# Kernel optimization log

Hardware: AMD Instinct MI355X
Metric: run time of the kernel (lower is better)

The kernel has to match this reference:

```python
import jax, jax.numpy as jnp
import numpy as np

DIM = 1024
HEADS = 16


def setup_inputs() -> dict:
    key = jax.random.key(0)
    k1, k2, k3, k4 = jax.random.split(key, 4)
    x = jax.random.normal(k1, (4, 2048, DIM), dtype=jnp.float32)
    # torch nn.Linear weights: [out_features, in_features]
    w_qkv = jax.random.normal(k2, (3 * DIM, DIM), dtype=jnp.float32) * (DIM ** -0.5)
    w_out = jax.random.normal(k3, (DIM, DIM), dtype=jnp.float32) * (DIM ** -0.5)
    b_out = jax.random.normal(k4, (DIM,), dtype=jnp.float32) * 0.01
    return {"x": x, "w_qkv": w_qkv, "w_out": w_out, "b_out": b_out}


def reference(x, w_qkv, w_out, b_out):
    b, n, d = x.shape
    h = HEADS
    hd = d // h
    scale = d ** -0.5  # note: full dim, matching the original module
    qkv = jnp.einsum('bnd,ed->bne', x, w_qkv)  # [b, n, 3d]
    q, k, v = jnp.split(qkv, 3, axis=-1)
    def to_heads(t):
        return t.reshape(b, n, h, hd).transpose(0, 2, 1, 3)  # [b, h, n, hd]
    q, k, v = map(to_heads, (q, k, v))
    dots = jnp.einsum('bhqd,bhkd->bhqk', q, k) * scale  # [b, h, n, n]
    attn = jax.nn.softmax(dots, axis=-1)
    out = jnp.einsum('bhqk,bhkd->bhqd', attn, v)  # [b, h, n, hd]
    out = out.transpose(0, 2, 1, 3).reshape(b, n, d)
    return jnp.einsum('bnd,ed->bne', out, w_out) + b_out
```

## Files before the change

### kernel.cpp

```cpp
#include <hip/hip_runtime.h>
#include <stdint.h>

#define SEQ   2048
#define NDIM  1024
#define NH    16
#define HD    64
#define KDIM  1024

typedef short  short8  __attribute__((ext_vector_type(8)));
typedef float  floatx4 __attribute__((ext_vector_type(4)));
typedef unsigned short ushort4v __attribute__((ext_vector_type(4)));
typedef _Float16 half8 __attribute__((ext_vector_type(8)));
typedef __fp16  fp16x2 __attribute__((ext_vector_type(2)));
typedef unsigned int uint2v __attribute__((ext_vector_type(2)));
typedef unsigned int uint4v __attribute__((ext_vector_type(4)));

typedef __attribute__((address_space(1))) void GV;
typedef __attribute__((address_space(3))) void LV;

#define QSCALE 0.04508422003f

__device__ __forceinline__ unsigned short f2bf(float f) {
    unsigned int u = __float_as_uint(f);
    u += 0x7fffu + ((u >> 16) & 1u);
    return (unsigned short)(u >> 16);
}

__device__ __forceinline__ float ex2(float x) {
#if __has_builtin(__builtin_amdgcn_exp2f)
    return __builtin_amdgcn_exp2f(x);
#else
    return exp2f(x);
#endif
}

__global__ __launch_bounds__(256) void cast_f32_bf16(const float* __restrict__ in,
                                                     unsigned short* __restrict__ out) {
    int i = (blockIdx.x * 256 + threadIdx.x) * 4;
    float4 v = *(const float4*)(in + i);
    ushort4v o;
    o.x = f2bf(v.x); o.y = f2bf(v.y); o.z = f2bf(v.z); o.w = f2bf(v.w);
    *(ushort4v*)(out + i) = o;
}

template<int MODE>
__global__ __launch_bounds__(256, 3)
void gemm_bt(const unsigned short* __restrict__ A,
             const unsigned short* __restrict__ B,
             unsigned short* __restrict__ Cq,
             unsigned short* __restrict__ Ck,
             unsigned short* __restrict__ Cv,
             const float* __restrict__ bias,
             float* __restrict__ Cout)
{
    __shared__ unsigned short As[2][4096];
    __shared__ unsigned short Bs[2][4096];
    const int tid  = threadIdx.x;
    const int lane = tid & 63;
    const int w    = tid >> 6;
    const int quad = lane >> 4;
    const int l15  = lane & 15;
    const int wm   = w >> 1, wn = w & 1;
    const int bm   = blockIdx.x, bn = blockIdx.y;

    const unsigned short* Arow = A + (size_t)bm * 128 * KDIM;
    const unsigned short* Brow = B + (size_t)bn * 128 * KDIM;

    const unsigned short* ga[2]; const unsigned short* gb[2];
    unsigned short* la[2][2];    unsigned short* lb[2][2];
#pragma unroll
    for (int i = 0; i < 2; ++i) {
        int j = ((w * 2 + i) << 6) + lane;
        int r = j >> 2;
        int c = (j & 3) ^ ((r >> 1) & 3);
        ga[i] = Arow + r * KDIM + c * 8;
        gb[i] = Brow + r * KDIM + c * 8;
#pragma unroll
        for (int b = 0; b < 2; ++b) {
            la[b][i] = &As[b][(w * 2 + i) << 9];
            lb[b][i] = &Bs[b][(w * 2 + i) << 9];
        }
    }

    int achunk[4], bchunk[4];
#pragma unroll
    for (int t = 0; t < 4; ++t) {
        int ra = wm * 64 + t * 16 + l15;
        achunk[t] = (ra << 2) + (quad ^ ((ra >> 1) & 3));
        int rb = wn * 64 + t * 16 + l15;
        bchunk[t] = (rb << 2) + (quad ^ ((rb >> 1) & 3));
    }

    floatx4 acc[4][4];
#pragma unroll
    for (int mt = 0; mt < 4; ++mt)
#pragma unroll
        for (int nt = 0; nt < 4; ++nt)
            acc[mt][nt] = (floatx4){0.f, 0.f, 0.f, 0.f};

#pragma unroll
    for (int i = 0; i < 2; ++i) {
        __builtin_amdgcn_global_load_lds((GV*)(void*)ga[i], (LV*)(void*)la[0][i], 16, 0, 0);
        __builtin_amdgcn_global_load_lds((GV*)(void*)gb[i], (LV*)(void*)lb[0][i], 16, 0, 0);
    }

    for (int kt = 0; kt < KDIM / 32; ++kt) {
        const int buf = kt & 1;
        __syncthreads();
        if (kt < KDIM / 32 - 1) {
#pragma unroll
            for (int i = 0; i < 2; ++i) {
                __builtin_amdgcn_global_load_lds((GV*)(void*)(ga[i] + (kt + 1) * 32), (LV*)(void*)la[buf ^ 1][i], 16, 0, 0);
                __builtin_amdgcn_global_load_lds((GV*)(void*)(gb[i] + (kt + 1) * 32), (LV*)(void*)lb[buf ^ 1][i], 16, 0, 0);
            }
        }
        short8 af[4], bf[4];
#pragma unroll
        for (int t = 0; t < 4; ++t) {
            af[t] = *(const short8*)(&As[buf][0] + (achunk[t] << 3));
            bf[t] = *(const short8*)(&Bs[buf][0] + (bchunk[t] << 3));
        }
#pragma unroll
        for (int mt = 0; mt < 4; ++mt)
#pragma unroll
            for (int nt = 0; nt < 4; ++nt)
                acc[mt][nt] = __builtin_amdgcn_mfma_f32_16x16x32_bf16(af[mt], bf[nt], acc[mt][nt], 0, 0, 0);
    }

    if (MODE == 0) {
        const int which = bn >> 3;
        unsigned short* dst = which == 0 ? Cq : (which == 1 ? Ck : Cv);
        if (which == 2) {
#pragma unroll
            for (int nt = 0; nt < 4; ++nt) {
                int e0   = ((bn & 7) << 7) + wn * 64 + nt * 16;
                int head = e0 >> 6;
                int hdi  = (e0 & 63) + l15;
#pragma unroll
                for (int mt = 0; mt < 4; ++mt) {
                    int n0 = bm * 128 + wm * 64 + mt * 16 + quad * 4;
                    int b  = n0 >> 11;
                    int n  = n0 & 2047;
                    int bh = (b << 4) + head;
                    int u  = (n & 127) >> 5;
                    size_t base = (size_t)bh * 131072
                                + (size_t)(n >> 7) * 8192
                                + (size_t)(u * 4 + ((hdi >> 4) & 3)) * 512
                                + (quad * 16 + (hdi & 15)) * 8
                                + ((mt & 1) << 2);
                    fp16x2 p01 = __builtin_amdgcn_cvt_pkrtz(acc[mt][nt][0], acc[mt][nt][1]);
                    fp16x2 p23 = __builtin_amdgcn_cvt_pkrtz(acc[mt][nt][2], acc[mt][nt][3]);
                    uint2v st;
                    st.x = __builtin_bit_cast(unsigned int, p01);
                    st.y = __builtin_bit_cast(unsigned int, p23);
                    *(uint2v*)(dst + base) = st;
                }
            }
        } else {
#pragma unroll
            for (int nt = 0; nt < 4; ++nt) {
                int e0   = ((bn & 7) << 7) + wn * 64 + nt * 16;
                int head = e0 >> 6;
                int hdi  = (e0 & 63) + l15;
#pragma unroll
                for (int mt = 0; mt < 4; ++mt) {
#pragma unroll
                    for (int r = 0; r < 4; ++r) {
                        int m = bm * 128 + wm * 64 + mt * 16 + quad * 4 + r;
                        int b = m >> 11, n = m & 2047;
                        int bh = (b << 4) + head;
                        float val = acc[mt][nt][r];
                        if (which == 0) {
                            dst[((size_t)bh * SEQ + n) * HD + hdi] = f2bf(val * QSCALE);
                        } else {
                            size_t idx = (size_t)bh * 131072
                                       + (size_t)(n >> 7) * 8192
                                       + (size_t)((((n >> 4) & 7) * 2) + (hdi >> 5)) * 512
                                       + ((((hdi >> 3) & 3) * 16) + (n & 15)) * 8
                                       + (hdi & 7);
                            dst[idx] = f2bf(val);
                        }
                    }
                }
            }
        }
    } else {
#pragma unroll
        for (int nt = 0; nt < 4; ++nt) {
            int e = bn * 128 + wn * 64 + nt * 16 + l15;
            float bv = bias[e];
#pragma unroll
            for (int mt = 0; mt < 4; ++mt) {
#pragma unroll
                for (int r = 0; r < 4; ++r) {
                    int m = bm * 128 + wm * 64 + mt * 16 + quad * 4 + r;
                    Cout[(size_t)m * NDIM + e] = acc[mt][nt][r] + bv;
                }
            }
        }
    }
}

__global__ __launch_bounds__(256, 4)
void attn_fused(const unsigned short* __restrict__ qb,
                const unsigned short* __restrict__ kfrag,
                const unsigned short* __restrict__ vfrag,
                unsigned short* __restrict__ ob)
{
    __shared__ unsigned short Ks[2][4096];
    __shared__ unsigned short Vs[2][4096];

    const int tid  = threadIdx.x;
    const int lane = tid & 63;
    const int w    = tid >> 6;
    const int quad = lane >> 4;
    const int l15  = lane & 15;

    const int bid  = blockIdx.x;
    const int xcd  = bid & 7;
    const int slot = bid >> 3;
    const int bh   = xcd * 8 + (slot >> 4);
    const int q0   = (slot & 15) * 128;

    const unsigned short* Qb = qb    + (size_t)bh * SEQ * HD;
    const unsigned short* Kb = kfrag + (size_t)bh * 131072;
    const unsigned short* Vb = vfrag + (size_t)bh * 131072;

    short8 qf[2][2];
#pragma unroll
    for (int qt = 0; qt < 2; ++qt)
#pragma unroll
        for (int ks = 0; ks < 2; ++ks)
            qf[qt][ks] = *(const short8*)(Qb + (size_t)(q0 + w * 32 + qt * 16 + l15) * HD + ks * 32 + quad * 8);

    floatx4 oacc[2][4];
    floatx4 lacc4[2];
#pragma unroll
    for (int qt = 0; qt < 2; ++qt) {
#pragma unroll
        for (int nt = 0; nt < 4; ++nt) oacc[qt][nt] = (floatx4){0.f, 0.f, 0.f, 0.f};
        lacc4[qt] = (floatx4){0.f, 0.f, 0.f, 0.f};
    }
    half8 vones;
#pragma unroll
    for (int i = 0; i < 8; ++i) vones[i] = (_Float16)1.0f;

    const unsigned short* gk[2]; const unsigned short* gv[2];
    unsigned short* lk[2][2];    unsigned short* lv[2][2];
#pragma unroll
    for (int i = 0; i < 2; ++i) {
        int off = (((w * 2 + i) << 6) + lane) * 8;
        gk[i] = Kb + off;
        gv[i] = Vb + off;
#pragma unroll
        for (int b = 0; b < 2; ++b) {
            lk[b][i] = &Ks[b][(w * 2 + i) << 9];
            lv[b][i] = &Vs[b][(w * 2 + i) << 9];
        }
    }

#pragma unroll
    for (int i = 0; i < 2; ++i) {
        __builtin_amdgcn_global_load_lds((GV*)(void*)gk[i], (LV*)(void*)lk[0][i], 16, 0, 0);
        __builtin_amdgcn_global_load_lds((GV*)(void*)gv[i], (LV*)(void*)lv[0][i], 16, 0, 0);
    }

    for (int t = 0; t < 32; ++t) {
        const int buf = t & 1;
        __syncthreads();
        if (t < 31) {
#pragma unroll
            for (int i = 0; i < 2; ++i) {
                __builtin_amdgcn_global_load_lds((GV*)(void*)(gk[i] + (t + 1) * 4096), (LV*)(void*)lk[buf ^ 1][i], 16, 0, 0);
                __builtin_amdgcn_global_load_lds((GV*)(void*)(gv[i] + (t + 1) * 4096), (LV*)(void*)lv[buf ^ 1][i], 16, 0, 0);
            }
        }
        const unsigned short* KsB = Ks[buf];
        const unsigned short* VsB = Vs[buf];

        floatx4 sacc[2][4];
#pragma unroll
        for (int qt = 0; qt < 2; ++qt)
#pragma unroll
            for (int nt = 0; nt < 4; ++nt) sacc[qt][nt] = (floatx4){0.f, 0.f, 0.f, 0.f};
#pragma unroll
        for (int ks = 0; ks < 2; ++ks) {
#pragma unroll
            for (int nt = 0; nt < 4; ++nt) {
                short8 kf = *(const short8*)(KsB + (nt * 2 + ks) * 512 + lane * 8);
                sacc[0][nt] = __builtin_amdgcn_mfma_f32_16x16x32_bf16(kf, qf[0][ks], sacc[0][nt], 0, 0, 0);
                sacc[1][nt] = __builtin_amdgcn_mfma_f32_16x16x32_bf16(kf, qf[1][ks], sacc[1][nt], 0, 0, 0);
            }
        }

#pragma unroll
        for (int u = 0; u < 2; ++u) {
            half8 pf[2];
#pragma unroll
            for (int qt = 0; qt < 2; ++qt) {
                floatx4 s0 = sacc[qt][2 * u];
                floatx4 s1 = sacc[qt][2 * u + 1];
                fp16x2 c0 = __builtin_amdgcn_cvt_pkrtz(ex2(s0[0]), ex2(s0[1]));
                fp16x2 c1 = __builtin_amdgcn_cvt_pkrtz(ex2(s0[2]), ex2(s0[3]));
                fp16x2 c2 = __builtin_amdgcn_cvt_pkrtz(ex2(s1[0]), ex2(s1[1]));
                fp16x2 c3 = __builtin_amdgcn_cvt_pkrtz(ex2(s1[2]), ex2(s1[3]));
                uint4v uu;
                uu.x = __builtin_bit_cast(unsigned int, c0);
                uu.y = __builtin_bit_cast(unsigned int, c1);
                uu.z = __builtin_bit_cast(unsigned int, c2);
                uu.w = __builtin_bit_cast(unsigned int, c3);
                pf[qt] = __builtin_bit_cast(half8, uu);
                lacc4[qt] = __builtin_amdgcn_mfma_f32_16x16x32_f16(pf[qt], vones, lacc4[qt], 0, 0, 0);
            }
#pragma unroll
            for (int nt = 0; nt < 4; ++nt) {
                uint4v vv = *(const uint4v*)(VsB + (u * 4 + nt) * 512 + lane * 8);
                half8 vf = __builtin_bit_cast(half8, vv);
                oacc[0][nt] = __builtin_amdgcn_mfma_f32_16x16x32_f16(pf[0], vf, oacc[0][nt], 0, 0, 0);
                oacc[1][nt] = __builtin_amdgcn_mfma_f32_16x16x32_f16(pf[1], vf, oacc[1][nt], 0, 0, 0);
            }
        }
    }

    const int b = bh >> 4, h = bh & 15;
#pragma unroll
    for (int qt = 0; qt < 2; ++qt) {
#pragma unroll
        for (int r = 0; r < 4; ++r) {
            float inv = 1.f / lacc4[qt][r];
            int n = q0 + w * 32 + qt * 16 + quad * 4 + r;
            size_t rowoff = ((size_t)b * SEQ + n) * NDIM + h * HD;
#pragma unroll
            for (int nt = 0; nt < 4; ++nt)
                ob[rowoff + nt * 16 + l15] = f2bf(oacc[qt][nt][r] * inv);
        }
    }
}

extern "C" void kernel_launch(void* const* d_in, const int* in_sizes, int n_in,
                              void* d_out, int out_size, void* d_ws, size_t ws_size,
                              hipStream_t stream)
{
    (void)in_sizes; (void)n_in; (void)out_size; (void)ws_size;
    const float* x    = (const float*)d_in[0];
    const float* wqkv = (const float*)d_in[1];
    const float* wout = (const float*)d_in[2];
    const float* bout = (const float*)d_in[3];
    float* out = (float*)d_out;

    unsigned short* xb    = (unsigned short*)d_ws;
    unsigned short* wqkvb = xb    + 8388608;
    unsigned short* woutb = wqkvb + 3145728;
    unsigned short* qbuf  = woutb + 1048576;
    unsigned short* kbuf  = qbuf  + 8388608;
    unsigned short* vbuf  = kbuf  + 8388608;
    unsigned short* obuf  = vbuf  + 8388608;

    cast_f32_bf16<<<8192, 256, 0, stream>>>(x, xb);
    cast_f32_bf16<<<3072, 256, 0, stream>>>(wqkv, wqkvb);
    cast_f32_bf16<<<1024, 256, 0, stream>>>(wout, woutb);

    gemm_bt<0><<<dim3(64, 24), 256, 0, stream>>>(xb, wqkvb, qbuf, kbuf, vbuf, nullptr, nullptr);
    attn_fused<<<1024, 256, 0, stream>>>(qbuf, kbuf, vbuf, obuf);
    gemm_bt<1><<<dim3(64, 8), 256, 0, stream>>>(obuf, woutb, nullptr, nullptr, nullptr, bout, out);
}
```

Before: 264.1 us.

## Split attention block across eight waves of sixteen query rows each

The attention kernel now launches 512 threads per block instead of 256. Each wave owns 16 query rows instead of 32, and each wave issues one K and one V async global-to-LDS copy per tile instead of two. Register use per wave roughly halves and launch bounds are raised to allow more resident waves, with s_setprio raised around the MFMA bursts to favour matrix issue. In exchange, every K/V fragment read from LDS now feeds half as many MFMAs, so LDS read traffic per FLOP doubles, and the tighter register cap may cause spills.

New measurement: 270.3 us. 2.3% more time.

```diff
diff --git a/kernel.cpp b/kernel.cpp
--- a/kernel.cpp
+++ b/kernel.cpp
@@ -201,7 +201,7 @@
     }
 }
 
-__global__ __launch_bounds__(256, 4)
+__global__ __launch_bounds__(512, 8)
 void attn_fused(const unsigned short* __restrict__ qb,
                 const unsigned short* __restrict__ kfrag,
                 const unsigned short* __restrict__ vfrag,
@@ -226,114 +226,89 @@
     const unsigned short* Kb = kfrag + (size_t)bh * 131072;
     const unsigned short* Vb = vfrag + (size_t)bh * 131072;
 
-    short8 qf[2][2];
-#pragma unroll
-    for (int qt = 0; qt < 2; ++qt)
-#pragma unroll
-        for (int ks = 0; ks < 2; ++ks)
-            qf[qt][ks] = *(const short8*)(Qb + (size_t)(q0 + w * 32 + qt * 16 + l15) * HD + ks * 32 + quad * 8);
-
-    floatx4 oacc[2][4];
-    floatx4 lacc4[2];
-#pragma unroll
-    for (int qt = 0; qt < 2; ++qt) {
-#pragma unroll
-        for (int nt = 0; nt < 4; ++nt) oacc[qt][nt] = (floatx4){0.f, 0.f, 0.f, 0.f};
-        lacc4[qt] = (floatx4){0.f, 0.f, 0.f, 0.f};
-    }
+    short8 qf[2];
+#pragma unroll
+    for (int ks = 0; ks < 2; ++ks)
+        qf[ks] = *(const short8*)(Qb + (size_t)(q0 + w * 16 + l15) * HD + ks * 32 + quad * 8);
+
+    floatx4 oacc[4];
+#pragma unroll
+    for (int nt = 0; nt < 4; ++nt) oacc[nt] = (floatx4){0.f, 0.f, 0.f, 0.f};
+    floatx4 lacc = (floatx4){0.f, 0.f, 0.f, 0.f};
+
     half8 vones;
 #pragma unroll
     for (int i = 0; i < 8; ++i) vones[i] = (_Float16)1.0f;
 
-    const unsigned short* gk[2]; const unsigned short* gv[2];
-    unsigned short* lk[2][2];    unsigned short* lv[2][2];
-#pragma unroll
-    for (int i = 0; i < 2; ++i) {
-        int off = (((w * 2 + i) << 6) + lane) * 8;
-        gk[i] = Kb + off;
-        gv[i] = Vb + off;
-#pragma unroll
-        for (int b = 0; b < 2; ++b) {
-            lk[b][i] = &Ks[b][(w * 2 + i) << 9];
-            lv[b][i] = &Vs[b][(w * 2 + i) << 9];
-        }
-    }
-
-#pragma unroll
-    for (int i = 0; i < 2; ++i) {
-        __builtin_amdgcn_global_load_lds((GV*)(void*)gk[i], (LV*)(void*)lk[0][i], 16, 0, 0);
-        __builtin_amdgcn_global_load_lds((GV*)(void*)gv[i], (LV*)(void*)lv[0][i], 16, 0, 0);
-    }
+    const unsigned short* gk = Kb + (size_t)((w << 6) + lane) * 8;
+    const unsigned short* gv = Vb + (size_t)((w << 6) + lane) * 8;
+    unsigned short* lk[2] = { &Ks[0][w << 9], &Ks[1][w << 9] };
+    unsigned short* lv[2] = { &Vs[0][w << 9], &Vs[1][w << 9] };
+
+    __builtin_amdgcn_global_load_lds((GV*)(void*)gk, (LV*)(void*)lk[0], 16, 0, 0);
+    __builtin_amdgcn_global_load_lds((GV*)(void*)gv, (LV*)(void*)lv[0], 16, 0, 0);
 
     for (int t = 0; t < 32; ++t) {
         const int buf = t & 1;
         __syncthreads();
         if (t < 31) {
-#pragma unroll
-            for (int i = 0; i < 2; ++i) {
-                __builtin_amdgcn_global_load_lds((GV*)(void*)(gk[i] + (t + 1) * 4096), (LV*)(void*)lk[buf ^ 1][i], 16, 0, 0);
-                __builtin_amdgcn_global_load_lds((GV*)(void*)(gv[i] + (t + 1) * 4096), (LV*)(void*)lv[buf ^ 1][i], 16, 0, 0);
-            }
+            __builtin_amdgcn_global_load_lds((GV*)(void*)(gk + (t + 1) * 4096), (LV*)(void*)lk[buf ^ 1], 16, 0, 0);
+            __builtin_amdgcn_global_load_lds((GV*)(void*)(gv + (t + 1) * 4096), (LV*)(void*)lv[buf ^ 1], 16, 0, 0);
         }
         const unsigned short* KsB = Ks[buf];
         const unsigned short* VsB = Vs[buf];
 
-        floatx4 sacc[2][4];
-#pragma unroll
-        for (int qt = 0; qt < 2; ++qt)
-#pragma unroll
-            for (int nt = 0; nt < 4; ++nt) sacc[qt][nt] = (floatx4){0.f, 0.f, 0.f, 0.f};
+        floatx4 sacc[4];
+#pragma unroll
+        for (int nt = 0; nt < 4; ++nt) sacc[nt] = (floatx4){0.f, 0.f, 0.f, 0.f};
+
+        __builtin_amdgcn_s_setprio(1);
 #pragma unroll
         for (int ks = 0; ks < 2; ++ks) {
 #pragma unroll
             for (int nt = 0; nt < 4; ++nt) {
                 short8 kf = *(const short8*)(KsB + (nt * 2 + ks) * 512 + lane * 8);
-                sacc[0][nt] = __builtin_amdgcn_mfma_f32_16x16x32_bf16(kf, qf[0][ks], sacc[0][nt], 0, 0, 0);
-                sacc[1][nt] = __builtin_amdgcn_mfma_f32_16x16x32_bf16(kf, qf[1][ks], sacc[1][nt], 0, 0, 0);
-            }
-        }
+                sacc[nt] = __builtin_amdgcn_mfma_f32_16x16x32_bf16(kf, qf[ks], sacc[nt], 0, 0, 0);
+            }
+        }
+        __builtin_amdgcn_s_setprio(0);
 
 #pragma unroll
         for (int u = 0; u < 2; ++u) {
-            half8 pf[2];
-#pragma unroll
-            for (int qt = 0; qt < 2; ++qt) {
-                floatx4 s0 = sacc[qt][2 * u];
-                floatx4 s1 = sacc[qt][2 * u + 1];
-                fp16x2 c0 = __builtin_amdgcn_cvt_pkrtz(ex2(s0[0]), ex2(s0[1]));
-                fp16x2 c1 = __builtin_amdgcn_cvt_pkrtz(ex2(s0[2]), ex2(s0[3]));
-                fp16x2 c2 = __builtin_amdgcn_cvt_pkrtz(ex2(s1[0]), ex2(s1[1]));
-                fp16x2 c3 = __builtin_amdgcn_cvt_pkrtz(ex2(s1[2]), ex2(s1[3]));
-                uint4v uu;
-                uu.x = __builtin_bit_cast(unsigned int, c0);
-                uu.y = __builtin_bit_cast(unsigned int, c1);
-                uu.z = __builtin_bit_cast(unsigned int, c2);
-                uu.w = __builtin_bit_cast(unsigned int, c3);
-                pf[qt] = __builtin_bit_cast(half8, uu);
-                lacc4[qt] = __builtin_amdgcn_mfma_f32_16x16x32_f16(pf[qt], vones, lacc4[qt], 0, 0, 0);
-            }
+            floatx4 s0 = sacc[2 * u];
+            floatx4 s1 = sacc[2 * u + 1];
+            fp16x2 c0 = __builtin_amdgcn_cvt_pkrtz(ex2(s0[0]), ex2(s0[1]));
+            fp16x2 c1 = __builtin_amdgcn_cvt_pkrtz(ex2(s0[2]), ex2(s0[3]));
+            fp16x2 c2 = __builtin_amdgcn_cvt_pkrtz(ex2(s1[0]), ex2(s1[1]));
+            fp16x2 c3 = __builtin_amdgcn_cvt_pkrtz(ex2(s1[2]), ex2(s1[3]));
+            uint4v uu;
+            uu.x = __builtin_bit_cast(unsigned int, c0);
+            uu.y = __builtin_bit_cast(unsigned int, c1);
+            uu.z = __builtin_bit_cast(unsigned int, c2);
+            uu.w = __builtin_bit_cast(unsigned int, c3);
+            half8 pf = __builtin_bit_cast(half8, uu);
+            lacc = __builtin_amdgcn_mfma_f32_16x16x32_f16(pf, vones, lacc, 0, 0, 0);
+
+            __builtin_amdgcn_s_setprio(1);
 #pragma unroll
             for (int nt = 0; nt < 4; ++nt) {
                 uint4v vv = *(const uint4v*)(VsB + (u * 4 + nt) * 512 + lane * 8);
                 half8 vf = __builtin_bit_cast(half8, vv);
-                oacc[0][nt] = __builtin_amdgcn_mfma_f32_16x16x32_f16(pf[0], vf, oacc[0][nt], 0, 0, 0);
-                oacc[1][nt] = __builtin_amdgcn_mfma_f32_16x16x32_f16(pf[1], vf, oacc[1][nt], 0, 0, 0);
-            }
+                oacc[nt] = __builtin_amdgcn_mfma_f32_16x16x32_f16(pf, vf, oacc[nt], 0, 0, 0);
+            }
+            __builtin_amdgcn_s_setprio(0);
         }
     }
 
     const int b = bh >> 4, h = bh & 15;
 #pragma unroll
-    for (int qt = 0; qt < 2; ++qt) {
-#pragma unroll
-        for (int r = 0; r < 4; ++r) {
-            float inv = 1.f / lacc4[qt][r];
-            int n = q0 + w * 32 + qt * 16 + quad * 4 + r;
-            size_t rowoff = ((size_t)b * SEQ + n) * NDIM + h * HD;
-#pragma unroll
-            for (int nt = 0; nt < 4; ++nt)
-                ob[rowoff + nt * 16 + l15] = f2bf(oacc[qt][nt][r] * inv);
-        }
+    for (int r = 0; r < 4; ++r) {
+        float inv = 1.f / lacc[r];
+        int n = q0 + w * 16 + quad * 4 + r;
+        size_t rowoff = ((size_t)b * SEQ + n) * NDIM + h * HD;
+#pragma unroll
+        for (int nt = 0; nt < 4; ++nt)
+            ob[rowoff + nt * 16 + l15] = f2bf(oacc[nt][r] * inv);
     }
 }
 
@@ -361,6 +336,6 @@
     cast_f32_bf16<<<1024, 256, 0, stream>>>(wout, woutb);
 
     gemm_bt<0><<<dim3(64, 24), 256, 0, stream>>>(xb, wqkvb, qbuf, kbuf, vbuf, nullptr, nullptr);
-    attn_fused<<<1024, 256, 0, stream>>>(qbuf, kbuf, vbuf, obuf);
+    attn_fused<<<1024, 512, 0, stream>>>(qbuf, kbuf, vbuf, obuf);
     gemm_bt<1><<<dim3(64, 8), 256, 0, stream>>>(obuf, woutb, nullptr, nullptr, nullptr, bout, out);
 }
```

## Switch attention to 32x32x16 MFMA with permlane32 swap and scalar row sums

Applied to the files above, without the earlier changes.

Rewrites the attention inner loop to use 32x32x16 MFMA tiles for both QK^T and PV, and re-lays out the K and V fragment buffers written by the QKV GEMM to match the new operand layout. The P fragments are rearranged in registers with v_permlane32_swap rather than going through memory. The softmax denominator is now accumulated with plain adds instead of an extra MFMA against a vector of ones, and s_setprio is raised around the MFMA sections. The aim is fewer MFMA issues and fewer LDS reads per tile, plus vectorized output stores, at the cost of larger accumulator register use and a tightly coupled layout across both kernels.

New measurement: 274.2 us. +3.8%, slower.

```diff
diff --git a/kernel.cpp b/kernel.cpp
--- a/kernel.cpp
+++ b/kernel.cpp
@@ -9,6 +9,7 @@
 
 typedef short  short8  __attribute__((ext_vector_type(8)));
 typedef float  floatx4 __attribute__((ext_vector_type(4)));
+typedef float  floatx16 __attribute__((ext_vector_type(16)));
 typedef unsigned short ushort4v __attribute__((ext_vector_type(4)));
 typedef _Float16 half8 __attribute__((ext_vector_type(8)));
 typedef __fp16  fp16x2 __attribute__((ext_vector_type(2)));
@@ -31,6 +32,15 @@
     return __builtin_amdgcn_exp2f(x);
 #else
     return exp2f(x);
+#endif
+}
+
+__device__ __forceinline__ void pl32swap(unsigned int &a, unsigned int &b) {
+#if __has_builtin(__builtin_amdgcn_permlane32_swap)
+    uint2v r = __builtin_amdgcn_permlane32_swap(a, b, false, false);
+    a = r.x; b = r.y;
+#else
+    asm("v_permlane32_swap_b32 %0, %1" : "+v"(a), "+v"(b));
 #endif
 }
 
@@ -135,19 +145,18 @@
             for (int nt = 0; nt < 4; ++nt) {
                 int e0   = ((bn & 7) << 7) + wn * 64 + nt * 16;
                 int head = e0 >> 6;
-                int hdi  = (e0 & 63) + l15;
+                int hd   = (e0 & 63) + l15;
 #pragma unroll
                 for (int mt = 0; mt < 4; ++mt) {
                     int n0 = bm * 128 + wm * 64 + mt * 16 + quad * 4;
                     int b  = n0 >> 11;
                     int n  = n0 & 2047;
                     int bh = (b << 4) + head;
-                    int u  = (n & 127) >> 5;
                     size_t base = (size_t)bh * 131072
-                                + (size_t)(n >> 7) * 8192
-                                + (size_t)(u * 4 + ((hdi >> 4) & 3)) * 512
-                                + (quad * 16 + (hdi & 15)) * 8
-                                + ((mt & 1) << 2);
+                                + (size_t)(n >> 6) * 4096
+                                + (size_t)((((hd >> 5) << 2) + ((n >> 4) & 3)) << 9)
+                                + ((((n >> 3) & 1) << 5) + (hd & 31)) * 8
+                                + (n & 7);
                     fp16x2 p01 = __builtin_amdgcn_cvt_pkrtz(acc[mt][nt][0], acc[mt][nt][1]);
                     fp16x2 p23 = __builtin_amdgcn_cvt_pkrtz(acc[mt][nt][2], acc[mt][nt][3]);
                     uint2v st;
@@ -161,7 +170,7 @@
             for (int nt = 0; nt < 4; ++nt) {
                 int e0   = ((bn & 7) << 7) + wn * 64 + nt * 16;
                 int head = e0 >> 6;
-                int hdi  = (e0 & 63) + l15;
+                int hd   = (e0 & 63) + l15;
 #pragma unroll
                 for (int mt = 0; mt < 4; ++mt) {
 #pragma unroll
@@ -171,13 +180,13 @@
                         int bh = (b << 4) + head;
                         float val = acc[mt][nt][r];
                         if (which == 0) {
-                            dst[((size_t)bh * SEQ + n) * HD + hdi] = f2bf(val * QSCALE);
+                            dst[((size_t)bh * SEQ + n) * HD + hd] = f2bf(val * QSCALE);
                         } else {
                             size_t idx = (size_t)bh * 131072
-                                       + (size_t)(n >> 7) * 8192
-                                       + (size_t)((((n >> 4) & 7) * 2) + (hdi >> 5)) * 512
-                                       + ((((hdi >> 3) & 3) * 16) + (n & 15)) * 8
-                                       + (hdi & 7);
+                                       + (size_t)(n >> 6) * 4096
+                                       + (size_t)(((((n >> 5) & 1) << 2) + (hd >> 4)) << 9)
+                                       + ((((hd >> 3) & 1) << 5) + (n & 31)) * 8
+                                       + (hd & 7);
                             dst[idx] = f2bf(val);
                         }
                     }
@@ -213,8 +222,8 @@
     const int tid  = threadIdx.x;
     const int lane = tid & 63;
     const int w    = tid >> 6;
-    const int quad = lane >> 4;
-    const int l15  = lane & 15;
+    const int l31  = lane & 31;
+    const int half = lane >> 5;
 
     const int bid  = blockIdx.x;
     const int xcd  = bid & 7;
@@ -226,24 +235,20 @@
     const unsigned short* Kb = kfrag + (size_t)bh * 131072;
     const unsigned short* Vb = vfrag + (size_t)bh * 131072;
 
-    short8 qf[2][2];
-#pragma unroll
-    for (int qt = 0; qt < 2; ++qt)
-#pragma unroll
-        for (int ks = 0; ks < 2; ++ks)
-            qf[qt][ks] = *(const short8*)(Qb + (size_t)(q0 + w * 32 + qt * 16 + l15) * HD + ks * 32 + quad * 8);
-
-    floatx4 oacc[2][4];
-    floatx4 lacc4[2];
-#pragma unroll
-    for (int qt = 0; qt < 2; ++qt) {
-#pragma unroll
-        for (int nt = 0; nt < 4; ++nt) oacc[qt][nt] = (floatx4){0.f, 0.f, 0.f, 0.f};
-        lacc4[qt] = (floatx4){0.f, 0.f, 0.f, 0.f};
-    }
-    half8 vones;
-#pragma unroll
-    for (int i = 0; i < 8; ++i) vones[i] = (_Float16)1.0f;
+    short8 qf[4];
+    {
+        const unsigned short* qrow = Qb + (size_t)(q0 + w * 32 + l31) * HD + half * 8;
+#pragma unroll
+        for (int ks = 0; ks < 4; ++ks)
+            qf[ks] = *(const short8*)(qrow + ks * 16);
+    }
+
+    floatx16 oacc[2];
+#pragma unroll
+    for (int ht = 0; ht < 2; ++ht)
+#pragma unroll
+        for (int i = 0; i < 16; ++i) oacc[ht][i] = 0.f;
+    float lp0 = 0.f, lp1 = 0.f, lp2 = 0.f, lp3 = 0.f;
 
     const unsigned short* gk[2]; const unsigned short* gv[2];
     unsigned short* lk[2][2];    unsigned short* lv[2][2];
@@ -278,61 +283,69 @@
         const unsigned short* KsB = Ks[buf];
         const unsigned short* VsB = Vs[buf];
 
-        floatx4 sacc[2][4];
-#pragma unroll
-        for (int qt = 0; qt < 2; ++qt)
-#pragma unroll
-            for (int nt = 0; nt < 4; ++nt) sacc[qt][nt] = (floatx4){0.f, 0.f, 0.f, 0.f};
-#pragma unroll
-        for (int ks = 0; ks < 2; ++ks) {
-#pragma unroll
-            for (int nt = 0; nt < 4; ++nt) {
-                short8 kf = *(const short8*)(KsB + (nt * 2 + ks) * 512 + lane * 8);
-                sacc[0][nt] = __builtin_amdgcn_mfma_f32_16x16x32_bf16(kf, qf[0][ks], sacc[0][nt], 0, 0, 0);
-                sacc[1][nt] = __builtin_amdgcn_mfma_f32_16x16x32_bf16(kf, qf[1][ks], sacc[1][nt], 0, 0, 0);
-            }
-        }
-
-#pragma unroll
-        for (int u = 0; u < 2; ++u) {
-            half8 pf[2];
-#pragma unroll
-            for (int qt = 0; qt < 2; ++qt) {
-                floatx4 s0 = sacc[qt][2 * u];
-                floatx4 s1 = sacc[qt][2 * u + 1];
-                fp16x2 c0 = __builtin_amdgcn_cvt_pkrtz(ex2(s0[0]), ex2(s0[1]));
-                fp16x2 c1 = __builtin_amdgcn_cvt_pkrtz(ex2(s0[2]), ex2(s0[3]));
-                fp16x2 c2 = __builtin_amdgcn_cvt_pkrtz(ex2(s1[0]), ex2(s1[1]));
-                fp16x2 c3 = __builtin_amdgcn_cvt_pkrtz(ex2(s1[2]), ex2(s1[3]));
-                uint4v uu;
-                uu.x = __builtin_bit_cast(unsigned int, c0);
-                uu.y = __builtin_bit_cast(unsigned int, c1);
-                uu.z = __builtin_bit_cast(unsigned int, c2);
-                uu.w = __builtin_bit_cast(unsigned int, c3);
-                pf[qt] = __builtin_bit_cast(half8, uu);
-                lacc4[qt] = __builtin_amdgcn_mfma_f32_16x16x32_f16(pf[qt], vones, lacc4[qt], 0, 0, 0);
-            }
-#pragma unroll
-            for (int nt = 0; nt < 4; ++nt) {
-                uint4v vv = *(const uint4v*)(VsB + (u * 4 + nt) * 512 + lane * 8);
-                half8 vf = __builtin_bit_cast(half8, vv);
-                oacc[0][nt] = __builtin_amdgcn_mfma_f32_16x16x32_f16(pf[0], vf, oacc[0][nt], 0, 0, 0);
-                oacc[1][nt] = __builtin_amdgcn_mfma_f32_16x16x32_f16(pf[1], vf, oacc[1][nt], 0, 0, 0);
-            }
-        }
-    }
-
+#pragma unroll
+        for (int kt = 0; kt < 2; ++kt) {
+            floatx16 s;
+#pragma unroll
+            for (int i = 0; i < 16; ++i) s[i] = 0.f;
+            __builtin_amdgcn_s_setprio(1);
+#pragma unroll
+            for (int ks = 0; ks < 4; ++ks) {
+                short8 kf = *(const short8*)(KsB + ((kt * 4 + ks) << 9) + lane * 8);
+                s = __builtin_amdgcn_mfma_f32_32x32x16_bf16(kf, qf[ks], s, 0, 0, 0);
+            }
+            __builtin_amdgcn_s_setprio(0);
+
+            float e[16];
+#pragma unroll
+            for (int i = 0; i < 16; ++i) e[i] = ex2(s[i]);
+            lp0 += (e[0] + e[1]) + (e[2] + e[3]);
+            lp1 += (e[4] + e[5]) + (e[6] + e[7]);
+            lp2 += (e[8] + e[9]) + (e[10] + e[11]);
+            lp3 += (e[12] + e[13]) + (e[14] + e[15]);
+            unsigned int u[8];
+#pragma unroll
+            for (int j = 0; j < 8; ++j) {
+                fp16x2 p = __builtin_amdgcn_cvt_pkrtz(e[2 * j], e[2 * j + 1]);
+                u[j] = __builtin_bit_cast(unsigned int, p);
+            }
+            pl32swap(u[0], u[2]); pl32swap(u[1], u[3]);
+            pl32swap(u[4], u[6]); pl32swap(u[5], u[7]);
+            half8 pb0, pb1;
+            { uint4v t0; t0.x = u[0]; t0.y = u[1]; t0.z = u[2]; t0.w = u[3];
+              pb0 = __builtin_bit_cast(half8, t0); }
+            { uint4v t1; t1.x = u[4]; t1.y = u[5]; t1.z = u[6]; t1.w = u[7];
+              pb1 = __builtin_bit_cast(half8, t1); }
+
+            __builtin_amdgcn_s_setprio(1);
+#pragma unroll
+            for (int ht = 0; ht < 2; ++ht) {
+                uint4v v0 = *(const uint4v*)(VsB + (((ht << 2) + kt * 2) << 9) + lane * 8);
+                uint4v v1 = *(const uint4v*)(VsB + (((ht << 2) + kt * 2 + 1) << 9) + lane * 8);
+                oacc[ht] = __builtin_amdgcn_mfma_f32_32x32x16_f16(__builtin_bit_cast(half8, v0), pb0, oacc[ht], 0, 0, 0);
+                oacc[ht] = __builtin_amdgcn_mfma_f32_32x32x16_f16(__builtin_bit_cast(half8, v1), pb1, oacc[ht], 0, 0, 0);
+            }
+            __builtin_amdgcn_s_setprio(0);
+        }
+    }
+
+    float lfull = (lp0 + lp1) + (lp2 + lp3);
+    lfull += __shfl_xor(lfull, 32);
+    float inv = 1.f / lfull;
     const int b = bh >> 4, h = bh & 15;
-#pragma unroll
-    for (int qt = 0; qt < 2; ++qt) {
-#pragma unroll
-        for (int r = 0; r < 4; ++r) {
-            float inv = 1.f / lacc4[qt][r];
-            int n = q0 + w * 32 + qt * 16 + quad * 4 + r;
-            size_t rowoff = ((size_t)b * SEQ + n) * NDIM + h * HD;
-#pragma unroll
-            for (int nt = 0; nt < 4; ++nt)
-                ob[rowoff + nt * 16 + l15] = f2bf(oacc[qt][nt][r] * inv);
+    const int qg = q0 + w * 32 + l31;
+    unsigned short* orow = ob + ((size_t)b * SEQ + qg) * NDIM + h * HD;
+#pragma unroll
+    for (int ht = 0; ht < 2; ++ht) {
+#pragma unroll
+        for (int g = 0; g < 4; ++g) {
+            int hd0 = ht * 32 + g * 8 + half * 4;
+            unsigned int w0 = (unsigned int)f2bf(oacc[ht][g * 4 + 0] * inv)
+                            | ((unsigned int)f2bf(oacc[ht][g * 4 + 1] * inv) << 16);
+            unsigned int w1 = (unsigned int)f2bf(oacc[ht][g * 4 + 2] * inv)
+                            | ((unsigned int)f2bf(oacc[ht][g * 4 + 3] * inv) << 16);
+            uint2v st; st.x = w0; st.y = w1;
+            *(uint2v*)(orow + hd0) = st;
         }
     }
 }
```
